# Kernel tuning notes

Measured on AMD Instinct MI355X. Metric: run time of the kernel, lower is better.

The kernel has to match this reference:

```python
import jax, jax.numpy as jnp
import numpy as np

N_NODES = 100000
N_EDGES = 1250000
D_IN = 64
D_H = 64
D_OUT = 32


def setup_inputs() -> dict:
    key = jax.random.key(0)
    ks = jax.random.split(key, 8)
    x = jax.random.normal(ks[0], (N_NODES, D_IN), dtype=jnp.float32)
    edge_index = jax.random.randint(ks[1], (2, N_EDGES), 0, N_NODES, dtype=jnp.int64)
    s = 0.1
    W1_l = jax.random.normal(ks[2], (D_H, D_IN), dtype=jnp.float32) * s
    W1_r = jax.random.normal(ks[3], (D_H, D_IN), dtype=jnp.float32) * s
    b1 = jnp.zeros((D_H,), dtype=jnp.float32)
    W2_l = jax.random.normal(ks[4], (D_OUT, D_H), dtype=jnp.float32) * s
    W2_r = jax.random.normal(ks[5], (D_OUT, D_H), dtype=jnp.float32) * s
    b2 = jnp.zeros((D_OUT,), dtype=jnp.float32)
    return {"x": x, "edge_index": edge_index, "W1_l": W1_l, "W1_r": W1_r,
            "b1": b1, "W2_l": W2_l, "W2_r": W2_r, "b2": b2}


def _sage_conv(x, src, dst, W_l, W_r, b):
    # PyG SAGEConv (aggr='mean', root_weight=True):
    #   out = lin_l(mean_{j in N(i)} x_j) + lin_r(x_i)
    n = x.shape[0]
    msg = x[src]                                            # [E, d] gather
    ssum = jax.ops.segment_sum(msg, dst, num_segments=n)    # [N, d]
    deg = jax.ops.segment_sum(jnp.ones((src.shape[0], 1), x.dtype), dst,
                              num_segments=n)               # [N, 1]
    mean = ssum / jnp.maximum(deg, 1.0)
    return mean @ W_l.T + b + x @ W_r.T


def reference(x, edge_index, W1_l, W1_r, b1, W2_l, W2_r, b2):
    src = edge_index[0]
    dst = edge_index[1]
    h = jax.nn.relu(_sage_conv(x, src, dst, W1_l, W1_r, b1))
    out = _sage_conv(h, src, dst, W2_l, W2_r, b2)
    return out
```

## Files before the change

### kernel.cpp

```cpp
#include <hip/hip_runtime.h>

#define N_NODES 100000
#define N_EDGES 1250000
#define D_IN 64
#define D_H 64
#define D_OUT 32

#define BUCKETS 196
#define GRP 512
#define PREP_NB 512
#define PREP_CH 2442
#define SCAP 48
#define BSTRIDE (PREP_NB*SCAP)
#define CSRCAP 8192

typedef __attribute__((ext_vector_type(8))) short bf16x8;
typedef __attribute__((ext_vector_type(4))) float f32x4;

__device__ __forceinline__ unsigned short f2bf(float f) {
    unsigned u = __float_as_uint(f);
    u = (u + 0x7fffu + ((u >> 16) & 1u)) >> 16;
    return (unsigned short)u;
}
__device__ __forceinline__ float bfhi(unsigned v) { return __uint_as_float(v & 0xffff0000u); }
__device__ __forceinline__ float bflo(unsigned v) { return __uint_as_float(v << 16); }


__global__ __launch_bounds__(256) void k_prep(const float* __restrict__ x,
                                              unsigned short* __restrict__ xh,
                                              const int* __restrict__ src,
                                              const int* __restrict__ dst,
                                              int* __restrict__ ebuf,
                                              int* __restrict__ pcnt) {
    __shared__ int ofs[BUCKETS];
    int t = threadIdx.x, b = blockIdx.x;
    for (int i = t; i < BUCKETS; i += 256) ofs[i] = 0;
    __syncthreads();

    const int TOT = N_NODES * 64 / 4;
    for (int i = b * 256 + t; i < TOT; i += PREP_NB * 256) {
        float4 v = *(const float4*)(x + (size_t)i * 4);
        uint2 u;
        u.x = (unsigned)f2bf(v.x) | ((unsigned)f2bf(v.y) << 16);
        u.y = (unsigned)f2bf(v.z) | ((unsigned)f2bf(v.w) << 16);
        *(uint2*)(xh + (size_t)i * 4) = u;
    }

    int e0 = b * PREP_CH;
    int e1 = e0 + PREP_CH; if (e1 > N_EDGES) e1 = N_EDGES;
    for (int e = e0 + t; e < e1; e += 256) {
        int s = src[e], d = dst[e];
        if ((unsigned)d >= N_NODES) continue;
        int sv = ((unsigned)s < N_NODES) ? s : 0;
        int bk = d >> 9;
        int r = atomicAdd(&ofs[bk], 1);
        if (r < SCAP) ebuf[bk * BSTRIDE + b * SCAP + r] = ((d & 511) << 17) | sv;
    }
    __syncthreads();
    for (int i = t; i < BUCKETS; i += 256) {
        int v = ofs[i]; if (v > SCAP) v = SCAP;
        pcnt[b * BUCKETS + i] = v;
    }
}

__global__ __launch_bounds__(256) void k_phb(const int* __restrict__ ebuf,
                                             const int* __restrict__ pcnt,
                                             int2* __restrict__ rd,
                                             int* __restrict__ csr_src) {
    __shared__ int sedge[CSRCAP];
    __shared__ int pc[PREP_NB];
    __shared__ int cnt[GRP];
    __shared__ int part[256];
    int b = blockIdx.x, t = threadIdx.x;

    int c0 = pcnt[(2 * t) * BUCKETS + b];
    int c1 = pcnt[(2 * t + 1) * BUCKETS + b];
    int s = c0 + c1;
    part[t] = s;
    __syncthreads();
    for (int off = 1; off < 256; off <<= 1) {
        int u = (t >= off) ? part[t - off] : 0;
        __syncthreads();
        part[t] += u;
        __syncthreads();
    }
    int run = part[t] - s;
    pc[2 * t] = run;
    pc[2 * t + 1] = run + c0;
    int n = part[255]; if (n > CSRCAP) n = CSRCAP;
    for (int i = t; i < GRP; i += 256) cnt[i] = 0;
    {
        const int* sp = ebuf + b * BSTRIDE + (2 * t) * SCAP;
        int base = pc[2 * t];
        for (int j = 0; j < c0; ++j) if (base + j < CSRCAP) sedge[base + j] = sp[j];
        sp += SCAP;
        base = pc[2 * t + 1];
        for (int j = 0; j < c1; ++j) if (base + j < CSRCAP) sedge[base + j] = sp[j];
    }
    __syncthreads();
    for (int i = t; i < n; i += 256) atomicAdd(&cnt[sedge[i] >> 17], 1);
    __syncthreads();
    int d0 = cnt[2 * t], d1 = cnt[2 * t + 1];
    int s2 = d0 + d1;
    part[t] = s2;
    __syncthreads();
    for (int off = 1; off < 256; off <<= 1) {
        int u = (t >= off) ? part[t - off] : 0;
        __syncthreads();
        part[t] += u;
        __syncthreads();
    }
    int g0 = b * CSRCAP + part[t] - s2;
    int node0 = b * GRP + 2 * t;
    if (node0 + 1 < N_NODES) {
        *(int4*)(rd + node0) = make_int4(g0, d0, g0 + d0, d1);
    } else if (node0 < N_NODES) {
        rd[node0] = make_int2(g0, d0);
    }
    __syncthreads();
    cnt[2 * t] = g0;
    cnt[2 * t + 1] = g0 + d0;
    __syncthreads();
    for (int i = t; i < n; i += 256) {
        int v = sedge[i];
        int pos = atomicAdd(&cnt[v >> 17], 1);
        csr_src[pos] = v & 0x1FFFF;
    }
}

__global__ __launch_bounds__(256) void k_gather1(
    const unsigned short* __restrict__ xh,
    const int2* __restrict__ rd,
    const int* __restrict__ csr_src,
    unsigned int* __restrict__ meanh)
{
    int lane = threadIdx.x & 63;
    int wv = threadIdx.x >> 6;
    int c = lane & 31;
    int hb = lane & 32;
    const unsigned* xp = (const unsigned*)xh;

    int node0 = blockIdx.x * 8 + wv * 2 + (hb >> 5);
    for (int row = node0; row < N_NODES; row += gridDim.x * 8) {
        int2 rdv = rd[row];
        int start = rdv.x, dg = rdv.y;
        int end = start + dg;
        float x0 = 0.f, y0 = 0.f, x1 = 0.f, y1 = 0.f;
        float x2 = 0.f, y2 = 0.f, x3 = 0.f, y3 = 0.f;
        float x4 = 0.f, y4 = 0.f, x5 = 0.f, y5 = 0.f;
        float x6 = 0.f, y6 = 0.f, x7 = 0.f, y7 = 0.f;
        for (int eb = start; eb < end; eb += 32) {
            int nv = end - eb; if (nv > 32) nv = 32;
            int sid = (c < nv) ? csr_src[eb + c] : 0;
            int j = 0;
            for (; j + 8 <= nv; j += 8) {
                int s0 = __shfl(sid, hb + j + 0, 64);
                int s1 = __shfl(sid, hb + j + 1, 64);
                int s2 = __shfl(sid, hb + j + 2, 64);
                int s3 = __shfl(sid, hb + j + 3, 64);
                int s4 = __shfl(sid, hb + j + 4, 64);
                int s5 = __shfl(sid, hb + j + 5, 64);
                int s6 = __shfl(sid, hb + j + 6, 64);
                int s7 = __shfl(sid, hb + j + 7, 64);
                unsigned v0 = xp[s0 * 32 + c];
                unsigned v1 = xp[s1 * 32 + c];
                unsigned v2 = xp[s2 * 32 + c];
                unsigned v3 = xp[s3 * 32 + c];
                unsigned v4 = xp[s4 * 32 + c];
                unsigned v5 = xp[s5 * 32 + c];
                unsigned v6 = xp[s6 * 32 + c];
                unsigned v7 = xp[s7 * 32 + c];
                x0 += bflo(v0); y0 += bfhi(v0);
                x1 += bflo(v1); y1 += bfhi(v1);
                x2 += bflo(v2); y2 += bfhi(v2);
                x3 += bflo(v3); y3 += bfhi(v3);
                x4 += bflo(v4); y4 += bfhi(v4);
                x5 += bflo(v5); y5 += bfhi(v5);
                x6 += bflo(v6); y6 += bfhi(v6);
                x7 += bflo(v7); y7 += bfhi(v7);
            }
            for (; j + 4 <= nv; j += 4) {
                int s0 = __shfl(sid, hb + j + 0, 64);
                int s1 = __shfl(sid, hb + j + 1, 64);
                int s2 = __shfl(sid, hb + j + 2, 64);
                int s3 = __shfl(sid, hb + j + 3, 64);
                unsigned v0 = xp[s0 * 32 + c];
                unsigned v1 = xp[s1 * 32 + c];
                unsigned v2 = xp[s2 * 32 + c];
                unsigned v3 = xp[s3 * 32 + c];
                x0 += bflo(v0); y0 += bfhi(v0);
                x1 += bflo(v1); y1 += bfhi(v1);
                x2 += bflo(v2); y2 += bfhi(v2);
                x3 += bflo(v3); y3 += bfhi(v3);
            }
            for (; j < nv; ++j) {
                int s = __shfl(sid, hb + j, 64);
                unsigned v = xp[s * 32 + c];
                x0 += bflo(v); y0 += bfhi(v);
            }
        }
        float rdeg = 1.0f / fmaxf((float)dg, 1.0f);
        float fx = (((x0 + x1) + (x2 + x3)) + ((x4 + x5) + (x6 + x7))) * rdeg;
        float fy = (((y0 + y1) + (y2 + y3)) + ((y4 + y5) + (y6 + y7))) * rdeg;
        meanh[(size_t)row * 32 + c] = (unsigned)f2bf(fx) | ((unsigned)f2bf(fy) << 16);
    }
}

__global__ __launch_bounds__(256) void k_gemm1(
    const unsigned short* __restrict__ xh, const unsigned short* __restrict__ meanh,
    const float* __restrict__ W1l, const float* __restrict__ W1r,
    const float* __restrict__ b1,
    const float* __restrict__ W2l, const float* __restrict__ W2r,
    unsigned short* __restrict__ hWlh, float* __restrict__ hr)
{
    __shared__ short sWB1[4 * 4 * 64 * 8];
    __shared__ short sWB2[2 * 4 * 64 * 8];
    __shared__ short htile[4][16 * 72];

    int tid = threadIdx.x;
    for (int e = tid; e < 1024; e += 256) {
        int kc = e >> 8, nt = (e >> 6) & 3, ln = e & 63;
        int cc = ln & 15, qd = ln >> 4;
        int n = nt * 16 + cc, k0 = kc * 32 + qd * 8;
        const float* sp = (k0 < 64) ? (W1l + n * 64 + k0) : (W1r + n * 64 + (k0 - 64));
        short* dp = sWB1 + e * 8;
        #pragma unroll
        for (int j = 0; j < 8; ++j) dp[j] = (short)f2bf(sp[j]);
    }
    for (int e = tid; e < 512; e += 256) {
        int kc = e >> 8, nt = (e >> 6) & 3, ln = e & 63;
        int cc = ln & 15, qd = ln >> 4;
        int n = nt * 16 + cc, k0 = kc * 32 + qd * 8;
        const float* sp = (n < 32) ? (W2l + n * 64 + k0) : (W2r + (n - 32) * 64 + k0);
        short* dp = sWB2 + e * 8;
        #pragma unroll
        for (int j = 0; j < 8; ++j) dp[j] = (short)f2bf(sp[j]);
    }
    __syncthreads();

    int lane = tid & 63, w = tid >> 6;
    int c = lane & 15, quad = lane >> 4;
    float bias[4];
    #pragma unroll
    for (int nt = 0; nt < 4; ++nt) bias[nt] = b1[nt * 16 + c];

    const bf16x8* B1 = (const bf16x8*)sWB1;
    const bf16x8* B2 = (const bf16x8*)sWB2;
    short* ht = htile[w];

    for (int r0 = blockIdx.x * 64 + w * 16; r0 < N_NODES; r0 += gridDim.x * 64) {
        int ra = r0 + c; if (ra > N_NODES - 1) ra = N_NODES - 1;
        const bf16x8* mrow = (const bf16x8*)((const unsigned short*)meanh + (size_t)ra * 64);
        const bf16x8* xrow = (const bf16x8*)(xh + (size_t)ra * 64);
        bf16x8 a0 = mrow[quad];
        bf16x8 a1 = mrow[4 + quad];
        bf16x8 a2 = xrow[quad];
        bf16x8 a3 = xrow[4 + quad];

        f32x4 acc[4];
        #pragma unroll
        for (int nt = 0; nt < 4; ++nt) acc[nt] = (f32x4){0.f, 0.f, 0.f, 0.f};
        #pragma unroll
        for (int nt = 0; nt < 4; ++nt)
            acc[nt] = __builtin_amdgcn_mfma_f32_16x16x32_bf16(a0, B1[(0 * 4 + nt) * 64 + lane], acc[nt], 0, 0, 0);
        #pragma unroll
        for (int nt = 0; nt < 4; ++nt)
            acc[nt] = __builtin_amdgcn_mfma_f32_16x16x32_bf16(a1, B1[(1 * 4 + nt) * 64 + lane], acc[nt], 0, 0, 0);
        #pragma unroll
        for (int nt = 0; nt < 4; ++nt)
            acc[nt] = __builtin_amdgcn_mfma_f32_16x16x32_bf16(a2, B1[(2 * 4 + nt) * 64 + lane], acc[nt], 0, 0, 0);
        #pragma unroll
        for (int nt = 0; nt < 4; ++nt)
            acc[nt] = __builtin_amdgcn_mfma_f32_16x16x32_bf16(a3, B1[(3 * 4 + nt) * 64 + lane], acc[nt], 0, 0, 0);

        #pragma unroll
        for (int nt = 0; nt < 4; ++nt) {
            #pragma unroll
            for (int reg = 0; reg < 4; ++reg) {
                float hv = fmaxf(acc[nt][reg] + bias[nt], 0.0f);
                ht[(quad * 4 + reg) * 72 + nt * 16 + c] = (short)f2bf(hv);
            }
        }
        bf16x8 h0 = *(const bf16x8*)(ht + c * 72 + 0  + quad * 8);
        bf16x8 h1 = *(const bf16x8*)(ht + c * 72 + 32 + quad * 8);

        f32x4 acc2[4];
        #pragma unroll
        for (int nt = 0; nt < 4; ++nt) acc2[nt] = (f32x4){0.f, 0.f, 0.f, 0.f};
        #pragma unroll
        for (int nt = 0; nt < 4; ++nt)
            acc2[nt] = __builtin_amdgcn_mfma_f32_16x16x32_bf16(h0, B2[(0 * 4 + nt) * 64 + lane], acc2[nt], 0, 0, 0);
        #pragma unroll
        for (int nt = 0; nt < 4; ++nt)
            acc2[nt] = __builtin_amdgcn_mfma_f32_16x16x32_bf16(h1, B2[(1 * 4 + nt) * 64 + lane], acc2[nt], 0, 0, 0);

        #pragma unroll
        for (int nt = 0; nt < 4; ++nt) {
            #pragma unroll
            for (int reg = 0; reg < 4; ++reg) {
                int row = r0 + quad * 4 + reg;
                if (row < N_NODES) {
                    if (nt < 2) hWlh[(size_t)row * 32 + nt * 16 + c] = f2bf(acc2[nt][reg]);
                    else        hr[(size_t)row * 32 + (nt - 2) * 16 + c] = acc2[nt][reg];
                }
            }
        }
    }
}

__global__ __launch_bounds__(256) void k_l2(
    const unsigned short* __restrict__ hWlh, const float* __restrict__ hr,
    const int2* __restrict__ rd,
    const int* __restrict__ csr_src,
    const float* __restrict__ b2, float* __restrict__ out)
{
    int lane = threadIdx.x & 63;
    int wv = threadIdx.x >> 6;
    int c = lane & 15;
    int qb = lane & 48;
    const unsigned* hp = (const unsigned*)hWlh;
    float2 b2v = ((const float2*)b2)[c];

    int node0 = blockIdx.x * 16 + wv * 4 + (qb >> 4);
    for (int row = node0; row < N_NODES; row += gridDim.x * 16) {
        int2 rdv = rd[row];
        int start = rdv.x, dg = rdv.y;
        int end = start + dg;
        float x0 = 0.f, y0 = 0.f, x1 = 0.f, y1 = 0.f;
        float x2 = 0.f, y2 = 0.f, x3 = 0.f, y3 = 0.f;
        float x4 = 0.f, y4 = 0.f, x5 = 0.f, y5 = 0.f;
        float x6 = 0.f, y6 = 0.f, x7 = 0.f, y7 = 0.f;
        for (int eb = start; eb < end; eb += 16) {
            int nv = end - eb; if (nv > 16) nv = 16;
            int sid = (c < nv) ? csr_src[eb + c] : 0;
            int j = 0;
            for (; j + 8 <= nv; j += 8) {
                int s0 = __shfl(sid, qb + j + 0, 64);
                int s1 = __shfl(sid, qb + j + 1, 64);
                int s2 = __shfl(sid, qb + j + 2, 64);
                int s3 = __shfl(sid, qb + j + 3, 64);
                int s4 = __shfl(sid, qb + j + 4, 64);
                int s5 = __shfl(sid, qb + j + 5, 64);
                int s6 = __shfl(sid, qb + j + 6, 64);
                int s7 = __shfl(sid, qb + j + 7, 64);
                unsigned v0 = hp[s0 * 16 + c];
                unsigned v1 = hp[s1 * 16 + c];
                unsigned v2 = hp[s2 * 16 + c];
                unsigned v3 = hp[s3 * 16 + c];
                unsigned v4 = hp[s4 * 16 + c];
                unsigned v5 = hp[s5 * 16 + c];
                unsigned v6 = hp[s6 * 16 + c];
                unsigned v7 = hp[s7 * 16 + c];
                x0 += bflo(v0); y0 += bfhi(v0);
                x1 += bflo(v1); y1 += bfhi(v1);
                x2 += bflo(v2); y2 += bfhi(v2);
                x3 += bflo(v3); y3 += bfhi(v3);
                x4 += bflo(v4); y4 += bfhi(v4);
                x5 += bflo(v5); y5 += bfhi(v5);
                x6 += bflo(v6); y6 += bfhi(v6);
                x7 += bflo(v7); y7 += bfhi(v7);
            }
            for (; j + 4 <= nv; j += 4) {
                int s0 = __shfl(sid, qb + j + 0, 64);
                int s1 = __shfl(sid, qb + j + 1, 64);
                int s2 = __shfl(sid, qb + j + 2, 64);
                int s3 = __shfl(sid, qb + j + 3, 64);
                unsigned v0 = hp[s0 * 16 + c];
                unsigned v1 = hp[s1 * 16 + c];
                unsigned v2 = hp[s2 * 16 + c];
                unsigned v3 = hp[s3 * 16 + c];
                x0 += bflo(v0); y0 += bfhi(v0);
                x1 += bflo(v1); y1 += bfhi(v1);
                x2 += bflo(v2); y2 += bfhi(v2);
                x3 += bflo(v3); y3 += bfhi(v3);
            }
            for (; j < nv; ++j) {
                int s = __shfl(sid, qb + j, 64);
                unsigned v = hp[s * 16 + c];
                x0 += bflo(v); y0 += bfhi(v);
            }
        }
        float fx = ((x0 + x1) + (x2 + x3)) + ((x4 + x5) + (x6 + x7));
        float fy = ((y0 + y1) + (y2 + y3)) + ((y4 + y5) + (y6 + y7));
        float rdeg = 1.0f / fmaxf((float)dg, 1.0f);
        float2 hv = ((const float2*)hr)[(size_t)row * 16 + c];
        float2 o;
        o.x = fmaf(fx, rdeg, hv.x + b2v.x);
        o.y = fmaf(fy, rdeg, hv.y + b2v.y);
        ((float2*)out)[(size_t)row * 16 + c] = o;
    }
}

extern "C" void kernel_launch(void* const* d_in, const int* in_sizes, int n_in,
                              void* d_out, int out_size, void* d_ws, size_t ws_size,
                              hipStream_t stream) {
    const float* x   = (const float*)d_in[0];
    const int*   ei  = (const int*)d_in[1];
    const float* W1l = (const float*)d_in[2];
    const float* W1r = (const float*)d_in[3];
    const float* b1  = (const float*)d_in[4];
    const float* W2l = (const float*)d_in[5];
    const float* W2r = (const float*)d_in[6];
    const float* b2  = (const float*)d_in[7];
    float* out = (float*)d_out;

    const int* src = ei;
    const int* dst = ei + N_EDGES;

    char* w = (char*)d_ws;
    int2* rd     = (int2*)w;  w += sizeof(int2) * (N_NODES + 4);
    int* pcnt    = (int*)w;   w += sizeof(int) * (PREP_NB * BUCKETS);
    int* csr_src = (int*)w;   w += sizeof(int) * (BUCKETS * CSRCAP);
    int* ebuf    = (int*)w;   w += sizeof(int) * (BUCKETS * BSTRIDE);
    unsigned short* xh    = (unsigned short*)w; w += sizeof(short) * (size_t)N_NODES * 64;
    unsigned int*   meanh = (unsigned int*)w;   w += sizeof(int)   * (size_t)N_NODES * 32;
    unsigned short* hWlh  = (unsigned short*)w; w += sizeof(short) * (size_t)N_NODES * 32;
    float*          hr    = (float*)w;

    k_prep<<<PREP_NB, 256, 0, stream>>>(x, xh, src, dst, ebuf, pcnt);
    k_phb<<<BUCKETS, 256, 0, stream>>>(ebuf, pcnt, rd, csr_src);
    k_gather1<<<4096, 256, 0, stream>>>(xh, rd, csr_src, meanh);
    k_gemm1<<<(N_NODES + 63) / 64, 256, 0, stream>>>(
        xh, (const unsigned short*)meanh, W1l, W1r, b1, W2l, W2r, hWlh, hr);
    k_l2<<<4096, 256, 0, stream>>>(hWlh, hr, rd, csr_src, b2, out);
}
```

Before: 201.6 us.

## Halve CSR bucket size, add nontemporal stores, store root term in bf16

Splits destinations into 391 buckets of 256 nodes, so each CSR-build block holds fewer edges, uses less shared memory and runs with one node per thread. Most global writes (bf16 features, edge buffer, CSR, intermediates, output) become nontemporal stores to reduce cache pollution. The layer-2 root term hr is stored as bf16 instead of fp32, halving its traffic at some cost in precision. Per-producer capacity shrinks from 48 to 32 edges per bucket, which raises the risk of silently dropping edges when a bucket is unusually full.

```diff
diff --git a/kernel.cpp b/kernel.cpp
--- a/kernel.cpp
+++ b/kernel.cpp
@@ -6,13 +6,13 @@
 #define D_H 64
 #define D_OUT 32
 
-#define BUCKETS 196
-#define GRP 512
+#define BUCKETS 391
+#define GRP 256
 #define PREP_NB 512
 #define PREP_CH 2442
-#define SCAP 48
+#define SCAP 32
 #define BSTRIDE (PREP_NB*SCAP)
-#define CSRCAP 8192
+#define CSRCAP 4096
 
 typedef __attribute__((ext_vector_type(8))) short bf16x8;
 typedef __attribute__((ext_vector_type(4))) float f32x4;
@@ -40,10 +40,10 @@
     const int TOT = N_NODES * 64 / 4;
     for (int i = b * 256 + t; i < TOT; i += PREP_NB * 256) {
         float4 v = *(const float4*)(x + (size_t)i * 4);
-        uint2 u;
-        u.x = (unsigned)f2bf(v.x) | ((unsigned)f2bf(v.y) << 16);
-        u.y = (unsigned)f2bf(v.z) | ((unsigned)f2bf(v.w) << 16);
-        *(uint2*)(xh + (size_t)i * 4) = u;
+        unsigned lo = (unsigned)f2bf(v.x) | ((unsigned)f2bf(v.y) << 16);
+        unsigned hi = (unsigned)f2bf(v.z) | ((unsigned)f2bf(v.w) << 16);
+        unsigned long long p = (unsigned long long)lo | ((unsigned long long)hi << 32);
+        __builtin_nontemporal_store(p, (unsigned long long*)(xh + (size_t)i * 4));
     }
 
     int e0 = b * PREP_CH;
@@ -52,9 +52,11 @@
         int s = src[e], d = dst[e];
         if ((unsigned)d >= N_NODES) continue;
         int sv = ((unsigned)s < N_NODES) ? s : 0;
-        int bk = d >> 9;
+        int bk = d >> 8;
         int r = atomicAdd(&ofs[bk], 1);
-        if (r < SCAP) ebuf[bk * BSTRIDE + b * SCAP + r] = ((d & 511) << 17) | sv;
+        if (r < SCAP)
+            __builtin_nontemporal_store(((d & 255) << 17) | sv,
+                                        &ebuf[bk * BSTRIDE + b * SCAP + r]);
     }
     __syncthreads();
     for (int i = t; i < BUCKETS; i += 256) {
@@ -68,7 +70,6 @@
                                              int2* __restrict__ rd,
                                              int* __restrict__ csr_src) {
     __shared__ int sedge[CSRCAP];
-    __shared__ int pc[PREP_NB];
     __shared__ int cnt[GRP];
     __shared__ int part[256];
     int b = blockIdx.x, t = threadIdx.x;
@@ -77,6 +78,7 @@
     int c1 = pcnt[(2 * t + 1) * BUCKETS + b];
     int s = c0 + c1;
     part[t] = s;
+    cnt[t] = 0;
     __syncthreads();
     for (int off = 1; off < 256; off <<= 1) {
         int u = (t >= off) ? part[t - off] : 0;
@@ -85,24 +87,20 @@
         __syncthreads();
     }
     int run = part[t] - s;
-    pc[2 * t] = run;
-    pc[2 * t + 1] = run + c0;
-    int n = part[255]; if (n > CSRCAP) n = CSRCAP;
-    for (int i = t; i < GRP; i += 256) cnt[i] = 0;
     {
         const int* sp = ebuf + b * BSTRIDE + (2 * t) * SCAP;
-        int base = pc[2 * t];
+        int base = run;
         for (int j = 0; j < c0; ++j) if (base + j < CSRCAP) sedge[base + j] = sp[j];
         sp += SCAP;
-        base = pc[2 * t + 1];
+        base = run + c0;
         for (int j = 0; j < c1; ++j) if (base + j < CSRCAP) sedge[base + j] = sp[j];
     }
+    int n = part[255]; if (n > CSRCAP) n = CSRCAP;
     __syncthreads();
     for (int i = t; i < n; i += 256) atomicAdd(&cnt[sedge[i] >> 17], 1);
     __syncthreads();
-    int d0 = cnt[2 * t], d1 = cnt[2 * t + 1];
-    int s2 = d0 + d1;
-    part[t] = s2;
+    int d0 = cnt[t];
+    part[t] = d0;
     __syncthreads();
     for (int off = 1; off < 256; off <<= 1) {
         int u = (t >= off) ? part[t - off] : 0;
@@ -110,21 +108,16 @@
         part[t] += u;
         __syncthreads();
     }
-    int g0 = b * CSRCAP + part[t] - s2;
-    int node0 = b * GRP + 2 * t;
-    if (node0 + 1 < N_NODES) {
-        *(int4*)(rd + node0) = make_int4(g0, d0, g0 + d0, d1);
-    } else if (node0 < N_NODES) {
-        rd[node0] = make_int2(g0, d0);
-    }
-    __syncthreads();
-    cnt[2 * t] = g0;
-    cnt[2 * t + 1] = g0 + d0;
+    int g0 = b * CSRCAP + part[t] - d0;
+    int node = b * GRP + t;
+    if (node < N_NODES) rd[node] = make_int2(g0, d0);
+    __syncthreads();
+    cnt[t] = g0;
     __syncthreads();
     for (int i = t; i < n; i += 256) {
         int v = sedge[i];
         int pos = atomicAdd(&cnt[v >> 17], 1);
-        csr_src[pos] = v & 0x1FFFF;
+        __builtin_nontemporal_store(v & 0x1FFFF, &csr_src[pos]);
     }
 }
 
@@ -202,7 +195,9 @@
         float rdeg = 1.0f / fmaxf((float)dg, 1.0f);
         float fx = (((x0 + x1) + (x2 + x3)) + ((x4 + x5) + (x6 + x7))) * rdeg;
         float fy = (((y0 + y1) + (y2 + y3)) + ((y4 + y5) + (y6 + y7))) * rdeg;
-        meanh[(size_t)row * 32 + c] = (unsigned)f2bf(fx) | ((unsigned)f2bf(fy) << 16);
+        __builtin_nontemporal_store(
+            (unsigned)f2bf(fx) | ((unsigned)f2bf(fy) << 16),
+            &meanh[(size_t)row * 32 + c]);
     }
 }
 
@@ -211,7 +206,7 @@
     const float* __restrict__ W1l, const float* __restrict__ W1r,
     const float* __restrict__ b1,
     const float* __restrict__ W2l, const float* __restrict__ W2r,
-    unsigned short* __restrict__ hWlh, float* __restrict__ hr)
+    unsigned short* __restrict__ hWlh, unsigned short* __restrict__ hrh)
 {
     __shared__ short sWB1[4 * 4 * 64 * 8];
     __shared__ short sWB2[2 * 4 * 64 * 8];
@@ -250,7 +245,7 @@
 
     for (int r0 = blockIdx.x * 64 + w * 16; r0 < N_NODES; r0 += gridDim.x * 64) {
         int ra = r0 + c; if (ra > N_NODES - 1) ra = N_NODES - 1;
-        const bf16x8* mrow = (const bf16x8*)((const unsigned short*)meanh + (size_t)ra * 64);
+        const bf16x8* mrow = (const bf16x8*)(meanh + (size_t)ra * 64);
         const bf16x8* xrow = (const bf16x8*)(xh + (size_t)ra * 64);
         bf16x8 a0 = mrow[quad];
         bf16x8 a1 = mrow[4 + quad];
@@ -300,8 +295,11 @@
             for (int reg = 0; reg < 4; ++reg) {
                 int row = r0 + quad * 4 + reg;
                 if (row < N_NODES) {
-                    if (nt < 2) hWlh[(size_t)row * 32 + nt * 16 + c] = f2bf(acc2[nt][reg]);
-                    else        hr[(size_t)row * 32 + (nt - 2) * 16 + c] = acc2[nt][reg];
+                    unsigned short q = f2bf(acc2[nt][reg]);
+                    if (nt < 2)
+                        __builtin_nontemporal_store(q, &hWlh[(size_t)row * 32 + nt * 16 + c]);
+                    else
+                        __builtin_nontemporal_store(q, &hrh[(size_t)row * 32 + (nt - 2) * 16 + c]);
                 }
             }
         }
@@ -309,7 +307,7 @@
 }
 
 __global__ __launch_bounds__(256) void k_l2(
-    const unsigned short* __restrict__ hWlh, const float* __restrict__ hr,
+    const unsigned short* __restrict__ hWlh, const unsigned short* __restrict__ hrh,
     const int2* __restrict__ rd,
     const int* __restrict__ csr_src,
     const float* __restrict__ b2, float* __restrict__ out)
@@ -318,7 +316,8 @@
     int wv = threadIdx.x >> 6;
     int c = lane & 15;
     int qb = lane & 48;
-    const unsigned* hp = (const unsigned*)hWlh;
+    const unsigned* hp  = (const unsigned*)hWlh;
+    const unsigned* hrp = (const unsigned*)hrh;
     float2 b2v = ((const float2*)b2)[c];
 
     int node0 = blockIdx.x * 16 + wv * 4 + (qb >> 4);
@@ -383,11 +382,11 @@
         float fx = ((x0 + x1) + (x2 + x3)) + ((x4 + x5) + (x6 + x7));
         float fy = ((y0 + y1) + (y2 + y3)) + ((y4 + y5) + (y6 + y7));
         float rdeg = 1.0f / fmaxf((float)dg, 1.0f);
-        float2 hv = ((const float2*)hr)[(size_t)row * 16 + c];
-        float2 o;
-        o.x = fmaf(fx, rdeg, hv.x + b2v.x);
-        o.y = fmaf(fy, rdeg, hv.y + b2v.y);
-        ((float2*)out)[(size_t)row * 16 + c] = o;
+        unsigned hru = hrp[(size_t)row * 16 + c];
+        float ox = fmaf(fx, rdeg, bflo(hru) + b2v.x);
+        float oy = fmaf(fy, rdeg, bfhi(hru) + b2v.y);
+        __builtin_nontemporal_store(ox, &out[(size_t)row * 32 + 2 * c]);
+        __builtin_nontemporal_store(oy, &out[(size_t)row * 32 + 2 * c + 1]);
     }
 }
 
@@ -411,16 +410,16 @@
     int2* rd     = (int2*)w;  w += sizeof(int2) * (N_NODES + 4);
     int* pcnt    = (int*)w;   w += sizeof(int) * (PREP_NB * BUCKETS);
     int* csr_src = (int*)w;   w += sizeof(int) * (BUCKETS * CSRCAP);
-    int* ebuf    = (int*)w;   w += sizeof(int) * (BUCKETS * BSTRIDE);
+    int* ebuf    = (int*)w;   w += sizeof(int) * ((size_t)BUCKETS * BSTRIDE);
     unsigned short* xh    = (unsigned short*)w; w += sizeof(short) * (size_t)N_NODES * 64;
     unsigned int*   meanh = (unsigned int*)w;   w += sizeof(int)   * (size_t)N_NODES * 32;
     unsigned short* hWlh  = (unsigned short*)w; w += sizeof(short) * (size_t)N_NODES * 32;
-    float*          hr    = (float*)w;
+    unsigned short* hrh   = (unsigned short*)w;
 
     k_prep<<<PREP_NB, 256, 0, stream>>>(x, xh, src, dst, ebuf, pcnt);
     k_phb<<<BUCKETS, 256, 0, stream>>>(ebuf, pcnt, rd, csr_src);
     k_gather1<<<4096, 256, 0, stream>>>(xh, rd, csr_src, meanh);
     k_gemm1<<<(N_NODES + 63) / 64, 256, 0, stream>>>(
-        xh, (const unsigned short*)meanh, W1l, W1r, b1, W2l, W2r, hWlh, hr);
-    k_l2<<<4096, 256, 0, stream>>>(hWlh, hr, rd, csr_src, b2, out);
-}
+        xh, (const unsigned short*)meanh, W1l, W1r, b1, W2l, W2r, hWlh, hrh);
+    k_l2<<<4096, 256, 0, stream>>>(hWlh, hrh, rd, csr_src, b2, out);
+}
```

New measurement: 241.6 us. +19.8%, slower.
